# Optimization experiments

Measured on AMD Instinct MI355X. Metric: run time of the kernel, lower is better.

## Reference

```python
import jax, jax.numpy as jnp
import numpy as np

N = 100000
E = 1600000
D_IN = 128
D_H = 128


def _sage_conv(x, src, dst, W_self, W_neigh, b, n_nodes):
    # mean aggregation over in-neighbors: dst receives from src
    gathered = x[src]                                        # [E, D]
    summed = jax.ops.segment_sum(gathered, dst, num_segments=n_nodes)  # [N, D]
    deg = jax.ops.segment_sum(jnp.ones((src.shape[0],), x.dtype), dst,
                              num_segments=n_nodes)          # [N]
    mean_neigh = summed / jnp.maximum(deg, 1.0)[:, None]     # zero-degree -> 0
    return x @ W_self + mean_neigh @ W_neigh + b


def setup_inputs() -> dict:
    key = jax.random.key(0)
    ks = jax.random.split(key, 9)
    s1 = 1.0 / np.sqrt(D_IN)
    s2 = 1.0 / np.sqrt(D_H)
    return {
        "in_feat": jax.random.normal(ks[0], (N, D_IN), jnp.float32),
        "W1_self": jax.random.uniform(ks[1], (D_IN, D_H), jnp.float32, -s1, s1),
        "W1_neigh": jax.random.uniform(ks[2], (D_IN, D_H), jnp.float32, -s1, s1),
        "b1": jnp.zeros((D_H,), jnp.float32),
        "W2_self": jax.random.uniform(ks[3], (D_H, D_H), jnp.float32, -s2, s2),
        "W2_neigh": jax.random.uniform(ks[4], (D_H, D_H), jnp.float32, -s2, s2),
        "b2": jnp.zeros((D_H,), jnp.float32),
        "src": jax.random.randint(ks[5], (E,), 0, N, jnp.int32),
        "dst": jax.random.randint(ks[6], (E,), 0, N, jnp.int32),
    }


def reference(in_feat, W1_self, W1_neigh, b1, W2_self, W2_neigh, b2, src, dst):
    h = _sage_conv(in_feat, src, dst, W1_self, W1_neigh, b1, N)
    h = jax.nn.relu(h)
    h = _sage_conv(h, src, dst, W2_self, W2_neigh, b2, N)
    return h
```

## Files before the change

### kernel.cpp

```cpp
#include <hip/hip_runtime.h>
#include <hip/hip_fp16.h>

#define D 128
#define NBK 512
#define CAP 4544
#define PART_CHUNK 3072

using f32x4  = __attribute__((ext_vector_type(4))) float;
using half8  = __attribute__((ext_vector_type(8))) _Float16;
using short8 = __attribute__((ext_vector_type(8))) short;

#define AS1(p) ((const __attribute__((address_space(1))) void*)(p))
#define AS3(p) ((__attribute__((address_space(3))) void*)(p))

#define FMA_MIX_LO(acc, dw, one) \
    asm("v_fma_mix_f32 %0, %1, %2, %0 op_sel:[0,0,0] op_sel_hi:[1,0,0]" \
        : "+v"(acc) : "v"(dw), "v"(one))
#define FMA_MIX_HI(acc, dw, one) \
    asm("v_fma_mix_f32 %0, %1, %2, %0 op_sel:[1,0,0] op_sel_hi:[1,0,0]" \
        : "+v"(acc) : "v"(dw), "v"(one))

__global__ void prep_k(const float* __restrict__ x, __half* __restrict__ y, int n4,
                       const float* __restrict__ W1s, const float* __restrict__ W1n,
                       const float* __restrict__ W2s, const float* __restrict__ W2n,
                       unsigned short* __restrict__ Wg1, unsigned short* __restrict__ Wg2,
                       float* __restrict__ xpad) {
    int b = blockIdx.x;
    int t = threadIdx.x;
    if (b < 256) {
        if (b == 0 && t < 64) xpad[t] = 0.f;
        int sel = b >> 7;
        int lb  = b & 127;
        const float* Ws = sel ? W2s : W1s;
        const float* Wn = sel ? W2n : W1n;
        unsigned short* Wg = sel ? Wg2 : Wg1;
        int idx = lb * 256 + t;
        int col = idx >> 8;
        int k   = idx & 255;
        float v = (k < 128) ? Ws[k * D + col] : Wn[(k - 128) * D + col];
        _Float16 hv = (_Float16)v;
        _Float16 lv = (_Float16)(v - (float)hv);
        int kc = k >> 5, q = (k >> 3) & 3, j = k & 7;
        Wg[(((kc * 2 + 0) * 4 + q) * 128 + col) * 8 + j] = *(unsigned short*)&hv;
        Wg[(((kc * 2 + 1) * 4 + q) * 128 + col) * 8 + j] = *(unsigned short*)&lv;
        return;
    }
    int i = (b - 256) * 256 + t;
    if (i < n4) {
        float4 v = *(const float4*)(x + (size_t)i * 4);
        __half2 h0 = __floats2half2_rn(v.x, v.y);
        __half2 h1 = __floats2half2_rn(v.z, v.w);
        __half2* o = (__half2*)(y + (size_t)i * 4);
        o[0] = h0; o[1] = h1;
    }
}

__global__ __launch_bounds__(256)
void partition_k(const int* __restrict__ src, const int* __restrict__ dst,
                 int* __restrict__ cursor, unsigned* __restrict__ pairs,
                 int E, int nb, int wmax) {
    __shared__ int hist[NBK];
    __shared__ int gbase[NBK];
    int t = threadIdx.x;
    int e0 = blockIdx.x * PART_CHUNK;
    int e1 = min(E, e0 + PART_CHUNK);
    int e1a = e0 + ((e1 - e0) & ~3);
    for (int b = t; b < nb; b += 256) hist[b] = 0;
    __syncthreads();
    for (int i = e0 + t * 4; i + 3 < e1; i += 1024) {
        int4 d4 = *(const int4*)(dst + i);
        atomicAdd(&hist[d4.x >> 8], 1);
        atomicAdd(&hist[d4.y >> 8], 1);
        atomicAdd(&hist[d4.z >> 8], 1);
        atomicAdd(&hist[d4.w >> 8], 1);
    }
    for (int i = e1a + t; i < e1; i += 256)
        atomicAdd(&hist[dst[i] >> 8], 1);
    __syncthreads();
    for (int b = t; b < nb; b += 256) {
        int c = hist[b];
        int g = b * CAP;
        if (c) g += atomicAdd(&cursor[b], c);
        gbase[b] = g;
        hist[b] = 0;
    }
    __syncthreads();
    for (int i = e0 + t * 4; i + 3 < e1; i += 1024) {
        int4 d4 = *(const int4*)(dst + i);
        int4 s4 = *(const int4*)(src + i);
        int b0 = d4.x >> 8, b1 = d4.y >> 8, b2 = d4.z >> 8, b3 = d4.w >> 8;
        int r0 = atomicAdd(&hist[b0], 1);
        int r1 = atomicAdd(&hist[b1], 1);
        int r2 = atomicAdd(&hist[b2], 1);
        int r3 = atomicAdd(&hist[b3], 1);
        pairs[min(gbase[b0] + r0, wmax)] = ((unsigned)(d4.x & 255) << 17) | (unsigned)s4.x;
        pairs[min(gbase[b1] + r1, wmax)] = ((unsigned)(d4.y & 255) << 17) | (unsigned)s4.y;
        pairs[min(gbase[b2] + r2, wmax)] = ((unsigned)(d4.z & 255) << 17) | (unsigned)s4.z;
        pairs[min(gbase[b3] + r3, wmax)] = ((unsigned)(d4.w & 255) << 17) | (unsigned)s4.w;
    }
    for (int i = e1a + t; i < e1; i += 256) {
        int dd = dst[i];
        int b = dd >> 8;
        int r = atomicAdd(&hist[b], 1);
        pairs[min(gbase[b] + r, wmax)] = ((unsigned)(dd & 255) << 17) | (unsigned)src[i];
    }
}

__global__ __launch_bounds__(1024)
void csr_agg_k(const __half* __restrict__ x, unsigned* pairs,
               const int* __restrict__ cursor, unsigned* __restrict__ offcnt,
               __half* __restrict__ agg, int n) {
    __shared__ int srcs[CAP];
    __shared__ int sh[256];
    __shared__ int hist[256];
    __shared__ int curs[256];
    __shared__ int soff[256];
    __shared__ int scnt[256];
    int t = threadIdx.x;
    int b = blockIdx.x;
    int e0 = b * CAP;
    int cnt = min(cursor[b], CAP);
    int e1 = e0 + cnt;
    if (t < 256) hist[t] = 0;
    __syncthreads();
    for (int i = e0 + t; i < e1; i += 1024)
        atomicAdd(&hist[pairs[i] >> 17], 1);
    __syncthreads();
    int c = 0;
    if (t < 256) { c = hist[t]; sh[t] = c; }
    __syncthreads();
    for (int off = 1; off < 256; off <<= 1) {
        int v = 0;
        if (t >= off && t < 256) v = sh[t - off];
        __syncthreads();
        if (t >= off && t < 256) sh[t] += v;
        __syncthreads();
    }
    if (t < 256) {
        int excl = sh[t] - c;
        curs[t] = excl;
        soff[t] = excl;
        scnt[t] = c;
        int node = (b << 8) + t;
        if (node < n)
            offcnt[node] = ((unsigned)(e0 + excl) << 9) | (unsigned)min(c, 511);
    }
    __syncthreads();
    for (int i = e0 + t; i < e1; i += 1024) {
        unsigned p = pairs[i];
        int pos = atomicAdd(&curs[p >> 17], 1);
        srcs[min(pos, CAP - 1)] = (int)(p & 0x1FFFFu);
    }
    __syncthreads();
    for (int i = t; i < cnt; i += 1024)
        pairs[e0 + i] = (unsigned)srcs[i];
    int lane = t & 63, wv = t >> 6;
    int sg = lane >> 4, sub = lane & 15;
    float one = 1.0f;
    for (int nl = wv; nl < 256; nl += 16) {
        int node = (b << 8) + nl;
        if (node >= n) break;
        int lstart = soff[nl];
        int cnt2 = scnt[nl];
        float acc[8] = {0.f, 0.f, 0.f, 0.f, 0.f, 0.f, 0.f, 0.f};
        for (int base = 0; base < cnt2; base += 64) {
            int valid = min(64, cnt2 - base);
            int s = (lane < valid) ? srcs[lstart + base + lane] : n;
            for (int k0 = 0; k0 < valid; k0 += 16) {
                float4 raw[4];
                #pragma unroll
                for (int u = 0; u < 4; ++u) {
                    int row = __shfl(s, (k0 + 4 * u + sg) & 63);
                    raw[u] = *(const float4*)(x + (size_t)row * D + sub * 8);
                }
                #pragma unroll
                for (int u = 0; u < 4; ++u) {
                    const unsigned* dw = (const unsigned*)&raw[u];
                    #pragma unroll
                    for (int j = 0; j < 4; ++j) {
                        FMA_MIX_LO(acc[2 * j],     dw[j], one);
                        FMA_MIX_HI(acc[2 * j + 1], dw[j], one);
                    }
                }
            }
        }
        #pragma unroll
        for (int j = 0; j < 8; ++j) {
            acc[j] += __shfl(acc[j], lane ^ 16);
            acc[j] += __shfl(acc[j], lane ^ 32);
        }
        if (sg == 0) {
            float inv = 1.0f / fmaxf((float)cnt2, 1.0f);
            union { __half2 h2[4]; short8 s8; } u8;
            #pragma unroll
            for (int j = 0; j < 4; ++j)
                u8.h2[j] = __floats2half2_rn(acc[2 * j] * inv, acc[2 * j + 1] * inv);
            *(short8*)(agg + (size_t)node * D + sub * 8) = u8.s8;
        }
    }
}

__global__ void aggregate_f16_k(const __half* __restrict__ x,
                                const int* __restrict__ edge_src,
                                const unsigned* __restrict__ offcnt,
                                __half* __restrict__ agg, int n) {
    int wid  = (blockIdx.x * blockDim.x + threadIdx.x) >> 6;
    int lane = threadIdx.x & 63;
    if (wid >= n) return;
    int sg  = lane >> 4;
    int sub = lane & 15;
    unsigned pc = offcnt[wid];
    int start = (int)(pc >> 9);
    int cnt   = (int)(pc & 511u);
    float one = 1.0f;
    float acc[8] = {0.f, 0.f, 0.f, 0.f, 0.f, 0.f, 0.f, 0.f};
    for (int base = 0; base < cnt; base += 64) {
        int valid = min(64, cnt - base);
        int s = (lane < valid) ? edge_src[start + base + lane] : n;
        for (int k0 = 0; k0 < valid; k0 += 16) {
            float4 raw[4];
            #pragma unroll
            for (int u = 0; u < 4; ++u) {
                int row = __shfl(s, (k0 + 4 * u + sg) & 63);
                raw[u] = *(const float4*)(x + (size_t)row * D + sub * 8);
            }
            #pragma unroll
            for (int u = 0; u < 4; ++u) {
                const unsigned* dw = (const unsigned*)&raw[u];
                #pragma unroll
                for (int j = 0; j < 4; ++j) {
                    FMA_MIX_LO(acc[2 * j],     dw[j], one);
                    FMA_MIX_HI(acc[2 * j + 1], dw[j], one);
                }
            }
        }
    }
    #pragma unroll
    for (int j = 0; j < 8; ++j) {
        acc[j] += __shfl(acc[j], lane ^ 16);
        acc[j] += __shfl(acc[j], lane ^ 32);
    }
    if (sg == 0) {
        float inv = 1.0f / fmaxf((float)cnt, 1.0f);
        union { __half2 h2[4]; short8 s8; } u;
        #pragma unroll
        for (int j = 0; j < 4; ++j)
            u.h2[j] = __floats2half2_rn(acc[2 * j] * inv, acc[2 * j + 1] * inv);
        *(short8*)(agg + (size_t)wid * D + sub * 8) = u.s8;
    }
}

__global__ __launch_bounds__(512)
void mfma_gemm_k(const _Float16* __restrict__ A0, const _Float16* __restrict__ A1,
                 const unsigned short* __restrict__ Wg,
                 const float* __restrict__ bias,
                 float* __restrict__ C, __half* __restrict__ Ch,
                 int n, int out_mode) {
    __shared__ __align__(16) unsigned short lds_b[8192];
    int t = threadIdx.x;
    int w = t >> 6;
    int l = t & 63;
    int m = l & 15;
    int q = l >> 4;
    int r0 = blockIdx.x * 256 + w * 32;

    f32x4 acc[2][8];
    #pragma unroll
    for (int rt = 0; rt < 2; ++rt)
        #pragma unroll
        for (int ct = 0; ct < 8; ++ct)
            acc[rt][ct] = (f32x4){0.f, 0.f, 0.f, 0.f};

    for (int kc = 0; kc < 8; ++kc) {
        const unsigned short* gk = Wg + (size_t)kc * 8192;
        #pragma unroll
        for (int i = 0; i < 2; ++i) {
            int e = i * 512 + t;
            __builtin_amdgcn_global_load_lds(AS1(gk + e * 8), AS3(lds_b + e * 8), 16, 0, 0);
        }
        const _Float16* __restrict__ A = (kc < 4) ? A0 : A1;
        int ka = (kc & 3) * 32;
        half8 a[2];
        #pragma unroll
        for (int rt = 0; rt < 2; ++rt) {
            int row = r0 + rt * 16 + m;
            half8 v = (half8){0, 0, 0, 0, 0, 0, 0, 0};
            if (row < n) v = *(const half8*)(A + (size_t)row * D + ka + q * 8);
            a[rt] = v;
        }
        __syncthreads();

        #pragma unroll
        for (int ct = 0; ct < 8; ++ct) {
            half8 bh = *(const half8*)&lds_b[(size_t)(q * 128 + ct * 16 + m) * 8];
            half8 bl = *(const half8*)&lds_b[(size_t)((4 + q) * 128 + ct * 16 + m) * 8];
            #pragma unroll
            for (int rt = 0; rt < 2; ++rt) {
                acc[rt][ct] = __builtin_amdgcn_mfma_f32_16x16x32_f16(a[rt], bh, acc[rt][ct], 0, 0, 0);
                acc[rt][ct] = __builtin_amdgcn_mfma_f32_16x16x32_f16(a[rt], bl, acc[rt][ct], 0, 0, 0);
            }
        }
        __syncthreads();
    }

    #pragma unroll
    for (int ct = 0; ct < 8; ++ct) {
        int col = ct * 16 + m;
        float bb = bias[col];
        #pragma unroll
        for (int rt = 0; rt < 2; ++rt) {
            #pragma unroll
            for (int r = 0; r < 4; ++r) {
                int row = r0 + rt * 16 + q * 4 + r;
                if (row < n) {
                    float v = acc[rt][ct][r] + bb;
                    if (out_mode) {
                        v = fmaxf(v, 0.f);
                        Ch[(size_t)row * D + col] = __float2half(v);
                    } else {
                        C[(size_t)row * D + col] = v;
                    }
                }
            }
        }
    }
}

extern "C" void kernel_launch(void* const* d_in, const int* in_sizes, int n_in,
                              void* d_out, int out_size, void* d_ws, size_t ws_size,
                              hipStream_t stream) {
    const float* in_feat = (const float*)d_in[0];
    const float* W1s     = (const float*)d_in[1];
    const float* W1n     = (const float*)d_in[2];
    const float* b1      = (const float*)d_in[3];
    const float* W2s     = (const float*)d_in[4];
    const float* W2n     = (const float*)d_in[5];
    const float* b2      = (const float*)d_in[6];
    const int*   src     = (const int*)d_in[7];
    const int*   dst     = (const int*)d_in[8];

    const int N  = in_sizes[0] / D;
    const int E  = in_sizes[7];
    const int NB = (N + 255) >> 8;

    char* base = (char*)d_ws;
    size_t off = 0;
    __half* agg16 = (__half*)(base + off); off += (size_t)N * D * 2;
    __half* xh16  = (__half*)(base + off); off += ((size_t)N * D + D) * 2;
    unsigned* pairs = (unsigned*)(base + off); off += (size_t)NB * CAP * 4;
    unsigned* offcnt = (unsigned*)(base + off); off += (size_t)N * 4;
    unsigned short* Wg1 = (unsigned short*)(base + off); off += 65536 * 2;
    unsigned short* Wg2 = (unsigned short*)(base + off); off += 65536 * 2;
    int* cursor = (int*)(base + off); off += NBK * 4;

    float* xpad = (float*)(xh16 + (size_t)N * D);

    const int n4 = (N * D) / 4;
    const int xb = (n4 + 255) / 256;
    const int pblk = (E + PART_CHUNK - 1) / PART_CHUNK;

    hipMemsetAsync(cursor, 0, NBK * 4, stream);

    hipLaunchKernelGGL(prep_k, dim3(256 + xb), dim3(256), 0, stream,
                       in_feat, xh16, n4, W1s, W1n, W2s, W2n, Wg1, Wg2, xpad);

    hipLaunchKernelGGL(partition_k, dim3(pblk), dim3(256), 0, stream,
                       src, dst, cursor, pairs, E, NB, NB * CAP - 1);

    const dim3 gemmGrid((N + 255) / 256);
    const dim3 aggGrid(((size_t)N * 64 + 255) / 256);

    hipLaunchKernelGGL(csr_agg_k, dim3(NB), dim3(1024), 0, stream,
                       xh16, pairs, cursor, offcnt, agg16, N);
    hipLaunchKernelGGL(mfma_gemm_k, gemmGrid, dim3(512), 0, stream,
                       (const _Float16*)xh16, (const _Float16*)agg16, Wg1, b1,
                       (float*)nullptr, xh16, N, 1);

    hipLaunchKernelGGL(aggregate_f16_k, aggGrid, dim3(256), 0, stream,
                       xh16, (const int*)pairs, offcnt, agg16, N);
    hipLaunchKernelGGL(mfma_gemm_k, gemmGrid, dim3(512), 0, stream,
                       (const _Float16*)xh16, (const _Float16*)agg16, Wg2, b2,
                       (float*)d_out, (__half*)nullptr, N, 0);
}
```

Baseline: 316.6 us.

## Fuse edge partition into prep kernel and cache pairs in registers in CSR build

```diff
diff --git a/kernel.cpp b/kernel.cpp
--- a/kernel.cpp
+++ b/kernel.cpp
@@ -4,7 +4,7 @@
 #define D 128
 #define NBK 512
 #define CAP 4544
-#define PART_CHUNK 3072
+#define PART_CHUNK 1536
 
 using f32x4  = __attribute__((ext_vector_type(4))) float;
 using half8  = __attribute__((ext_vector_type(8))) _Float16;
@@ -20,17 +20,69 @@
     asm("v_fma_mix_f32 %0, %1, %2, %0 op_sel:[1,0,0] op_sel_hi:[1,0,0]" \
         : "+v"(acc) : "v"(dw), "v"(one))
 
-__global__ void prep_k(const float* __restrict__ x, __half* __restrict__ y, int n4,
-                       const float* __restrict__ W1s, const float* __restrict__ W1n,
-                       const float* __restrict__ W2s, const float* __restrict__ W2n,
-                       unsigned short* __restrict__ Wg1, unsigned short* __restrict__ Wg2,
-                       float* __restrict__ xpad) {
+__global__ __launch_bounds__(256)
+void prep_part_k(const int* __restrict__ src, const int* __restrict__ dst,
+                 int* __restrict__ cursor, unsigned* __restrict__ pairs,
+                 int E, int nb, int wmax, int pblk,
+                 const float* __restrict__ x, __half* __restrict__ y, int n4,
+                 const float* __restrict__ W1s, const float* __restrict__ W1n,
+                 const float* __restrict__ W2s, const float* __restrict__ W2n,
+                 unsigned short* __restrict__ Wg1, unsigned short* __restrict__ Wg2,
+                 float* __restrict__ xpad) {
+    __shared__ int hist[NBK];
+    __shared__ int gbase[NBK];
     int b = blockIdx.x;
     int t = threadIdx.x;
-    if (b < 256) {
-        if (b == 0 && t < 64) xpad[t] = 0.f;
-        int sel = b >> 7;
-        int lb  = b & 127;
+    if (b < pblk) {
+        int e0 = b * PART_CHUNK;
+        int e1 = min(E, e0 + PART_CHUNK);
+        int e1a = e0 + ((e1 - e0) & ~3);
+        for (int i = t; i < nb; i += 256) hist[i] = 0;
+        __syncthreads();
+        for (int i = e0 + t * 4; i + 3 < e1; i += 1024) {
+            int4 d4 = *(const int4*)(dst + i);
+            atomicAdd(&hist[d4.x >> 8], 1);
+            atomicAdd(&hist[d4.y >> 8], 1);
+            atomicAdd(&hist[d4.z >> 8], 1);
+            atomicAdd(&hist[d4.w >> 8], 1);
+        }
+        for (int i = e1a + t; i < e1; i += 256)
+            atomicAdd(&hist[dst[i] >> 8], 1);
+        __syncthreads();
+        for (int i = t; i < nb; i += 256) {
+            int c = hist[i];
+            int g = i * CAP;
+            if (c) g += atomicAdd(&cursor[i], c);
+            gbase[i] = g;
+            hist[i] = 0;
+        }
+        __syncthreads();
+        for (int i = e0 + t * 4; i + 3 < e1; i += 1024) {
+            int4 d4 = *(const int4*)(dst + i);
+            int4 s4 = *(const int4*)(src + i);
+            int b0 = d4.x >> 8, b1 = d4.y >> 8, b2 = d4.z >> 8, b3 = d4.w >> 8;
+            int r0 = atomicAdd(&hist[b0], 1);
+            int r1 = atomicAdd(&hist[b1], 1);
+            int r2 = atomicAdd(&hist[b2], 1);
+            int r3 = atomicAdd(&hist[b3], 1);
+            pairs[min(gbase[b0] + r0, wmax)] = ((unsigned)(d4.x & 255) << 17) | (unsigned)s4.x;
+            pairs[min(gbase[b1] + r1, wmax)] = ((unsigned)(d4.y & 255) << 17) | (unsigned)s4.y;
+            pairs[min(gbase[b2] + r2, wmax)] = ((unsigned)(d4.z & 255) << 17) | (unsigned)s4.z;
+            pairs[min(gbase[b3] + r3, wmax)] = ((unsigned)(d4.w & 255) << 17) | (unsigned)s4.w;
+        }
+        for (int i = e1a + t; i < e1; i += 256) {
+            int dd = dst[i];
+            int bb = dd >> 8;
+            int r = atomicAdd(&hist[bb], 1);
+            pairs[min(gbase[bb] + r, wmax)] = ((unsigned)(dd & 255) << 17) | (unsigned)src[i];
+        }
+        return;
+    }
+    int wb = b - pblk;
+    if (wb < 256) {
+        if (wb == 0 && t < 64) xpad[t] = 0.f;
+        int sel = wb >> 7;
+        int lb  = wb & 127;
         const float* Ws = sel ? W2s : W1s;
         const float* Wn = sel ? W2n : W1n;
         unsigned short* Wg = sel ? Wg2 : Wg1;
@@ -45,64 +97,13 @@
         Wg[(((kc * 2 + 1) * 4 + q) * 128 + col) * 8 + j] = *(unsigned short*)&lv;
         return;
     }
-    int i = (b - 256) * 256 + t;
+    int i = (b - pblk - 256) * 256 + t;
     if (i < n4) {
         float4 v = *(const float4*)(x + (size_t)i * 4);
         __half2 h0 = __floats2half2_rn(v.x, v.y);
         __half2 h1 = __floats2half2_rn(v.z, v.w);
         __half2* o = (__half2*)(y + (size_t)i * 4);
         o[0] = h0; o[1] = h1;
-    }
-}
-
-__global__ __launch_bounds__(256)
-void partition_k(const int* __restrict__ src, const int* __restrict__ dst,
-                 int* __restrict__ cursor, unsigned* __restrict__ pairs,
-                 int E, int nb, int wmax) {
-    __shared__ int hist[NBK];
-    __shared__ int gbase[NBK];
-    int t = threadIdx.x;
-    int e0 = blockIdx.x * PART_CHUNK;
-    int e1 = min(E, e0 + PART_CHUNK);
-    int e1a = e0 + ((e1 - e0) & ~3);
-    for (int b = t; b < nb; b += 256) hist[b] = 0;
-    __syncthreads();
-    for (int i = e0 + t * 4; i + 3 < e1; i += 1024) {
-        int4 d4 = *(const int4*)(dst + i);
-        atomicAdd(&hist[d4.x >> 8], 1);
-        atomicAdd(&hist[d4.y >> 8], 1);
-        atomicAdd(&hist[d4.z >> 8], 1);
-        atomicAdd(&hist[d4.w >> 8], 1);
-    }
-    for (int i = e1a + t; i < e1; i += 256)
-        atomicAdd(&hist[dst[i] >> 8], 1);
-    __syncthreads();
-    for (int b = t; b < nb; b += 256) {
-        int c = hist[b];
-        int g = b * CAP;
-        if (c) g += atomicAdd(&cursor[b], c);
-        gbase[b] = g;
-        hist[b] = 0;
-    }
-    __syncthreads();
-    for (int i = e0 + t * 4; i + 3 < e1; i += 1024) {
-        int4 d4 = *(const int4*)(dst + i);
-        int4 s4 = *(const int4*)(src + i);
-        int b0 = d4.x >> 8, b1 = d4.y >> 8, b2 = d4.z >> 8, b3 = d4.w >> 8;
-        int r0 = atomicAdd(&hist[b0], 1);
-        int r1 = atomicAdd(&hist[b1], 1);
-        int r2 = atomicAdd(&hist[b2], 1);
-        int r3 = atomicAdd(&hist[b3], 1);
-        pairs[min(gbase[b0] + r0, wmax)] = ((unsigned)(d4.x & 255) << 17) | (unsigned)s4.x;
-        pairs[min(gbase[b1] + r1, wmax)] = ((unsigned)(d4.y & 255) << 17) | (unsigned)s4.y;
-        pairs[min(gbase[b2] + r2, wmax)] = ((unsigned)(d4.z & 255) << 17) | (unsigned)s4.z;
-        pairs[min(gbase[b3] + r3, wmax)] = ((unsigned)(d4.w & 255) << 17) | (unsigned)s4.w;
-    }
-    for (int i = e1a + t; i < e1; i += 256) {
-        int dd = dst[i];
-        int b = dd >> 8;
-        int r = atomicAdd(&hist[b], 1);
-        pairs[min(gbase[b] + r, wmax)] = ((unsigned)(dd & 255) << 17) | (unsigned)src[i];
     }
 }
 
@@ -123,8 +124,15 @@
     int e1 = e0 + cnt;
     if (t < 256) hist[t] = 0;
     __syncthreads();
-    for (int i = e0 + t; i < e1; i += 1024)
-        atomicAdd(&hist[pairs[i] >> 17], 1);
+    unsigned pr[5];
+    #pragma unroll
+    for (int j = 0; j < 5; ++j) {
+        int idx = e0 + j * 1024 + t;
+        pr[j] = (idx < e1) ? pairs[idx] : 0xFFFFFFFFu;
+    }
+    #pragma unroll
+    for (int j = 0; j < 5; ++j)
+        if (pr[j] != 0xFFFFFFFFu) atomicAdd(&hist[pr[j] >> 17], 1);
     __syncthreads();
     int c = 0;
     if (t < 256) { c = hist[t]; sh[t] = c; }
@@ -146,11 +154,12 @@
             offcnt[node] = ((unsigned)(e0 + excl) << 9) | (unsigned)min(c, 511);
     }
     __syncthreads();
-    for (int i = e0 + t; i < e1; i += 1024) {
-        unsigned p = pairs[i];
-        int pos = atomicAdd(&curs[p >> 17], 1);
-        srcs[min(pos, CAP - 1)] = (int)(p & 0x1FFFFu);
-    }
+    #pragma unroll
+    for (int j = 0; j < 5; ++j)
+        if (pr[j] != 0xFFFFFFFFu) {
+            int pos = atomicAdd(&curs[pr[j] >> 17], 1);
+            srcs[min(pos, CAP - 1)] = (int)(pr[j] & 0x1FFFFu);
+        }
     __syncthreads();
     for (int i = t; i < cnt; i += 1024)
         pairs[e0 + i] = (unsigned)srcs[i];
@@ -361,11 +370,9 @@
 
     hipMemsetAsync(cursor, 0, NBK * 4, stream);
 
-    hipLaunchKernelGGL(prep_k, dim3(256 + xb), dim3(256), 0, stream,
+    hipLaunchKernelGGL(prep_part_k, dim3(pblk + 256 + xb), dim3(256), 0, stream,
+                       src, dst, cursor, pairs, E, NB, NB * CAP - 1, pblk,
                        in_feat, xh16, n4, W1s, W1n, W2s, W2n, Wg1, Wg2, xpad);
-
-    hipLaunchKernelGGL(partition_k, dim3(pblk), dim3(256), 0, stream,
-                       src, dst, cursor, pairs, E, NB, NB * CAP - 1);
 
     const dim3 gemmGrid((N + 255) / 256);
     const dim3 aggGrid(((size_t)N * 64 + 255) / 256);
```

Measured after the change: 326.1 us. +3.0%, slower.

## Fuse neighbor aggregation with MFMA GEMM per 256-node block

Applied to the files above, without the earlier changes.

```diff
diff --git a/kernel.cpp b/kernel.cpp
--- a/kernel.cpp
+++ b/kernel.cpp
@@ -24,11 +24,11 @@
                        const float* __restrict__ W1s, const float* __restrict__ W1n,
                        const float* __restrict__ W2s, const float* __restrict__ W2n,
                        unsigned short* __restrict__ Wg1, unsigned short* __restrict__ Wg2,
-                       float* __restrict__ xpad) {
+                       float* __restrict__ xpad, float* __restrict__ hpad) {
     int b = blockIdx.x;
     int t = threadIdx.x;
     if (b < 256) {
-        if (b == 0 && t < 64) xpad[t] = 0.f;
+        if (b == 0 && t < 64) { xpad[t] = 0.f; hpad[t] = 0.f; }
         int sel = b >> 7;
         int lb  = b & 127;
         const float* Ws = sel ? W2s : W1s;
@@ -100,17 +100,22 @@
     }
     for (int i = e1a + t; i < e1; i += 256) {
         int dd = dst[i];
-        int b = dd >> 8;
-        int r = atomicAdd(&hist[b], 1);
-        pairs[min(gbase[b] + r, wmax)] = ((unsigned)(dd & 255) << 17) | (unsigned)src[i];
+        int bb = dd >> 8;
+        int r = atomicAdd(&hist[bb], 1);
+        pairs[min(gbase[bb] + r, wmax)] = ((unsigned)(dd & 255) << 17) | (unsigned)src[i];
     }
 }
 
 __global__ __launch_bounds__(1024)
-void csr_agg_k(const __half* __restrict__ x, unsigned* pairs,
-               const int* __restrict__ cursor, unsigned* __restrict__ offcnt,
-               __half* __restrict__ agg, int n) {
+void agg_gemm_k(const __half* __restrict__ xin, unsigned* pairs,
+                const int* __restrict__ cursor, unsigned* __restrict__ offcnt,
+                const unsigned short* __restrict__ Wg,
+                const float* __restrict__ bias,
+                __half* __restrict__ hout, float* __restrict__ fout,
+                int n, int layer1) {
     __shared__ int srcs[CAP];
+    __shared__ __align__(16) __half agg_lds[256][D + 8];
+    __shared__ __align__(16) unsigned short lds_b[8192];
     __shared__ int sh[256];
     __shared__ int hist[256];
     __shared__ int curs[256];
@@ -120,45 +125,65 @@
     int b = blockIdx.x;
     int e0 = b * CAP;
     int cnt = min(cursor[b], CAP);
-    int e1 = e0 + cnt;
-    if (t < 256) hist[t] = 0;
-    __syncthreads();
-    for (int i = e0 + t; i < e1; i += 1024)
-        atomicAdd(&hist[pairs[i] >> 17], 1);
-    __syncthreads();
-    int c = 0;
-    if (t < 256) { c = hist[t]; sh[t] = c; }
-    __syncthreads();
-    for (int off = 1; off < 256; off <<= 1) {
-        int v = 0;
-        if (t >= off && t < 256) v = sh[t - off];
-        __syncthreads();
-        if (t >= off && t < 256) sh[t] += v;
-        __syncthreads();
-    }
-    if (t < 256) {
-        int excl = sh[t] - c;
-        curs[t] = excl;
-        soff[t] = excl;
-        scnt[t] = c;
-        int node = (b << 8) + t;
-        if (node < n)
-            offcnt[node] = ((unsigned)(e0 + excl) << 9) | (unsigned)min(c, 511);
-    }
-    __syncthreads();
-    for (int i = e0 + t; i < e1; i += 1024) {
-        unsigned p = pairs[i];
-        int pos = atomicAdd(&curs[p >> 17], 1);
-        srcs[min(pos, CAP - 1)] = (int)(p & 0x1FFFFu);
-    }
-    __syncthreads();
-    for (int i = t; i < cnt; i += 1024)
-        pairs[e0 + i] = (unsigned)srcs[i];
+    int node0 = b << 8;
+    if (layer1) {
+        if (t < 256) hist[t] = 0;
+        __syncthreads();
+        unsigned pr[5];
+        #pragma unroll
+        for (int j = 0; j < 5; ++j) {
+            int idx = j * 1024 + t;
+            pr[j] = (idx < cnt) ? pairs[e0 + idx] : 0xFFFFFFFFu;
+        }
+        #pragma unroll
+        for (int j = 0; j < 5; ++j)
+            if (pr[j] != 0xFFFFFFFFu) atomicAdd(&hist[pr[j] >> 17], 1);
+        __syncthreads();
+        int c = 0;
+        if (t < 256) { c = hist[t]; sh[t] = c; }
+        __syncthreads();
+        for (int off = 1; off < 256; off <<= 1) {
+            int v = 0;
+            if (t >= off && t < 256) v = sh[t - off];
+            __syncthreads();
+            if (t >= off && t < 256) sh[t] += v;
+            __syncthreads();
+        }
+        if (t < 256) {
+            int excl = sh[t] - c;
+            curs[t] = excl;
+            soff[t] = excl;
+            scnt[t] = c;
+            int node = node0 + t;
+            if (node < n)
+                offcnt[node] = ((unsigned)excl << 9) | (unsigned)min(c, 511);
+        }
+        __syncthreads();
+        #pragma unroll
+        for (int j = 0; j < 5; ++j)
+            if (pr[j] != 0xFFFFFFFFu) {
+                int pos = atomicAdd(&curs[pr[j] >> 17], 1);
+                srcs[min(pos, CAP - 1)] = (int)(pr[j] & 0x1FFFFu);
+            }
+        __syncthreads();
+        for (int i = t; i < cnt; i += 1024)
+            pairs[e0 + i] = (unsigned)srcs[i];
+    } else {
+        for (int i = t; i < cnt; i += 1024)
+            srcs[i] = (int)pairs[e0 + i];
+        if (t < 256) {
+            int node = node0 + t;
+            unsigned pc = (node < n) ? offcnt[node] : 0u;
+            soff[t] = (int)(pc >> 9);
+            scnt[t] = (int)(pc & 511u);
+        }
+        __syncthreads();
+    }
     int lane = t & 63, wv = t >> 6;
     int sg = lane >> 4, sub = lane & 15;
     float one = 1.0f;
     for (int nl = wv; nl < 256; nl += 16) {
-        int node = (b << 8) + nl;
+        int node = node0 + nl;
         if (node >= n) break;
         int lstart = soff[nl];
         int cnt2 = scnt[nl];
@@ -171,7 +196,7 @@
                 #pragma unroll
                 for (int u = 0; u < 4; ++u) {
                     int row = __shfl(s, (k0 + 4 * u + sg) & 63);
-                    raw[u] = *(const float4*)(x + (size_t)row * D + sub * 8);
+                    raw[u] = *(const float4*)(xin + (size_t)row * D + sub * 8);
                 }
                 #pragma unroll
                 for (int u = 0; u < 4; ++u) {
@@ -195,131 +220,52 @@
             #pragma unroll
             for (int j = 0; j < 4; ++j)
                 u8.h2[j] = __floats2half2_rn(acc[2 * j] * inv, acc[2 * j + 1] * inv);
-            *(short8*)(agg + (size_t)node * D + sub * 8) = u8.s8;
-        }
-    }
-}
-
-__global__ void aggregate_f16_k(const __half* __restrict__ x,
-                                const int* __restrict__ edge_src,
-                                const unsigned* __restrict__ offcnt,
-                                __half* __restrict__ agg, int n) {
-    int wid  = (blockIdx.x * blockDim.x + threadIdx.x) >> 6;
-    int lane = threadIdx.x & 63;
-    if (wid >= n) return;
-    int sg  = lane >> 4;
-    int sub = lane & 15;
-    unsigned pc = offcnt[wid];
-    int start = (int)(pc >> 9);
-    int cnt   = (int)(pc & 511u);
-    float one = 1.0f;
-    float acc[8] = {0.f, 0.f, 0.f, 0.f, 0.f, 0.f, 0.f, 0.f};
-    for (int base = 0; base < cnt; base += 64) {
-        int valid = min(64, cnt - base);
-        int s = (lane < valid) ? edge_src[start + base + lane] : n;
-        for (int k0 = 0; k0 < valid; k0 += 16) {
-            float4 raw[4];
-            #pragma unroll
-            for (int u = 0; u < 4; ++u) {
-                int row = __shfl(s, (k0 + 4 * u + sg) & 63);
-                raw[u] = *(const float4*)(x + (size_t)row * D + sub * 8);
-            }
-            #pragma unroll
-            for (int u = 0; u < 4; ++u) {
-                const unsigned* dw = (const unsigned*)&raw[u];
-                #pragma unroll
-                for (int j = 0; j < 4; ++j) {
-                    FMA_MIX_LO(acc[2 * j],     dw[j], one);
-                    FMA_MIX_HI(acc[2 * j + 1], dw[j], one);
-                }
-            }
-        }
-    }
+            *(short8*)(&agg_lds[nl][sub * 8]) = u8.s8;
+        }
+    }
+    __syncthreads();
+    int m = lane & 15, q = lane >> 4;
+    int rowl = wv * 16 + m;
+    int rowg = node0 + rowl;
+    f32x4 acc2[8];
     #pragma unroll
-    for (int j = 0; j < 8; ++j) {
-        acc[j] += __shfl(acc[j], lane ^ 16);
-        acc[j] += __shfl(acc[j], lane ^ 32);
-    }
-    if (sg == 0) {
-        float inv = 1.0f / fmaxf((float)cnt, 1.0f);
-        union { __half2 h2[4]; short8 s8; } u;
-        #pragma unroll
-        for (int j = 0; j < 4; ++j)
-            u.h2[j] = __floats2half2_rn(acc[2 * j] * inv, acc[2 * j + 1] * inv);
-        *(short8*)(agg + (size_t)wid * D + sub * 8) = u.s8;
-    }
-}
-
-__global__ __launch_bounds__(512)
-void mfma_gemm_k(const _Float16* __restrict__ A0, const _Float16* __restrict__ A1,
-                 const unsigned short* __restrict__ Wg,
-                 const float* __restrict__ bias,
-                 float* __restrict__ C, __half* __restrict__ Ch,
-                 int n, int out_mode) {
-    __shared__ __align__(16) unsigned short lds_b[8192];
-    int t = threadIdx.x;
-    int w = t >> 6;
-    int l = t & 63;
-    int m = l & 15;
-    int q = l >> 4;
-    int r0 = blockIdx.x * 256 + w * 32;
-
-    f32x4 acc[2][8];
-    #pragma unroll
-    for (int rt = 0; rt < 2; ++rt)
-        #pragma unroll
-        for (int ct = 0; ct < 8; ++ct)
-            acc[rt][ct] = (f32x4){0.f, 0.f, 0.f, 0.f};
-
+    for (int ct = 0; ct < 8; ++ct) acc2[ct] = (f32x4){0.f, 0.f, 0.f, 0.f};
     for (int kc = 0; kc < 8; ++kc) {
         const unsigned short* gk = Wg + (size_t)kc * 8192;
-        #pragma unroll
-        for (int i = 0; i < 2; ++i) {
-            int e = i * 512 + t;
-            __builtin_amdgcn_global_load_lds(AS1(gk + e * 8), AS3(lds_b + e * 8), 16, 0, 0);
-        }
-        const _Float16* __restrict__ A = (kc < 4) ? A0 : A1;
+        __builtin_amdgcn_global_load_lds(AS1(gk + t * 8), AS3(lds_b + t * 8), 16, 0, 0);
         int ka = (kc & 3) * 32;
-        half8 a[2];
-        #pragma unroll
-        for (int rt = 0; rt < 2; ++rt) {
-            int row = r0 + rt * 16 + m;
-            half8 v = (half8){0, 0, 0, 0, 0, 0, 0, 0};
-            if (row < n) v = *(const half8*)(A + (size_t)row * D + ka + q * 8);
-            a[rt] = v;
-        }
-        __syncthreads();
-
+        half8 a;
+        if (kc < 4) {
+            a = (half8){0, 0, 0, 0, 0, 0, 0, 0};
+            if (rowg < n)
+                a = *(const half8*)((const _Float16*)xin + (size_t)rowg * D + ka + q * 8);
+        } else {
+            a = *(const half8*)(&agg_lds[rowl][ka + q * 8]);
+        }
+        __syncthreads();
         #pragma unroll
         for (int ct = 0; ct < 8; ++ct) {
             half8 bh = *(const half8*)&lds_b[(size_t)(q * 128 + ct * 16 + m) * 8];
             half8 bl = *(const half8*)&lds_b[(size_t)((4 + q) * 128 + ct * 16 + m) * 8];
-            #pragma unroll
-            for (int rt = 0; rt < 2; ++rt) {
-                acc[rt][ct] = __builtin_amdgcn_mfma_f32_16x16x32_f16(a[rt], bh, acc[rt][ct], 0, 0, 0);
-                acc[rt][ct] = __builtin_amdgcn_mfma_f32_16x16x32_f16(a[rt], bl, acc[rt][ct], 0, 0, 0);
-            }
-        }
-        __syncthreads();
-    }
-
+            acc2[ct] = __builtin_amdgcn_mfma_f32_16x16x32_f16(a, bh, acc2[ct], 0, 0, 0);
+            acc2[ct] = __builtin_amdgcn_mfma_f32_16x16x32_f16(a, bl, acc2[ct], 0, 0, 0);
+        }
+        __syncthreads();
+    }
     #pragma unroll
     for (int ct = 0; ct < 8; ++ct) {
         int col = ct * 16 + m;
         float bb = bias[col];
         #pragma unroll
-        for (int rt = 0; rt < 2; ++rt) {
-            #pragma unroll
-            for (int r = 0; r < 4; ++r) {
-                int row = r0 + rt * 16 + q * 4 + r;
-                if (row < n) {
-                    float v = acc[rt][ct][r] + bb;
-                    if (out_mode) {
-                        v = fmaxf(v, 0.f);
-                        Ch[(size_t)row * D + col] = __float2half(v);
-                    } else {
-                        C[(size_t)row * D + col] = v;
-                    }
+        for (int r = 0; r < 4; ++r) {
+            int row = node0 + wv * 16 + q * 4 + r;
+            if (row < n) {
+                float v = acc2[ct][r] + bb;
+                if (layer1) {
+                    v = fmaxf(v, 0.f);
+                    hout[(size_t)row * D + col] = __float2half(v);
+                } else {
+                    fout[(size_t)row * D + col] = v;
                 }
             }
         }
@@ -345,8 +291,8 @@
 
     char* base = (char*)d_ws;
     size_t off = 0;
-    __half* agg16 = (__half*)(base + off); off += (size_t)N * D * 2;
-    __half* xh16  = (__half*)(base + off); off += ((size_t)N * D + D) * 2;
+    __half* h16  = (__half*)(base + off); off += ((size_t)N * D + D) * 2;
+    __half* xh16 = (__half*)(base + off); off += ((size_t)N * D + D) * 2;
     unsigned* pairs = (unsigned*)(base + off); off += (size_t)NB * CAP * 4;
     unsigned* offcnt = (unsigned*)(base + off); off += (size_t)N * 4;
     unsigned short* Wg1 = (unsigned short*)(base + off); off += 65536 * 2;
@@ -354,6 +300,7 @@
     int* cursor = (int*)(base + off); off += NBK * 4;
 
     float* xpad = (float*)(xh16 + (size_t)N * D);
+    float* hpad = (float*)(h16  + (size_t)N * D);
 
     const int n4 = (N * D) / 4;
     const int xb = (n4 + 255) / 256;
@@ -362,23 +309,16 @@
     hipMemsetAsync(cursor, 0, NBK * 4, stream);
 
     hipLaunchKernelGGL(prep_k, dim3(256 + xb), dim3(256), 0, stream,
-                       in_feat, xh16, n4, W1s, W1n, W2s, W2n, Wg1, Wg2, xpad);
+                       in_feat, xh16, n4, W1s, W1n, W2s, W2n, Wg1, Wg2, xpad, hpad);
 
     hipLaunchKernelGGL(partition_k, dim3(pblk), dim3(256), 0, stream,
                        src, dst, cursor, pairs, E, NB, NB * CAP - 1);
 
-    const dim3 gemmGrid((N + 255) / 256);
-    const dim3 aggGrid(((size_t)N * 64 + 255) / 256);
-
-    hipLaunchKernelGGL(csr_agg_k, dim3(NB), dim3(1024), 0, stream,
-                       xh16, pairs, cursor, offcnt, agg16, N);
-    hipLaunchKernelGGL(mfma_gemm_k, gemmGrid, dim3(512), 0, stream,
-                       (const _Float16*)xh16, (const _Float16*)agg16, Wg1, b1,
-                       (float*)nullptr, xh16, N, 1);
-
-    hipLaunchKernelGGL(aggregate_f16_k, aggGrid, dim3(256), 0, stream,
-                       xh16, (const int*)pairs, offcnt, agg16, N);
-    hipLaunchKernelGGL(mfma_gemm_k, gemmGrid, dim3(512), 0, stream,
-                       (const _Float16*)xh16, (const _Float16*)agg16, Wg2, b2,
-                       (float*)d_out, (__half*)nullptr, N, 0);
+    hipLaunchKernelGGL(agg_gemm_k, dim3(NB), dim3(1024), 0, stream,
+                       xh16, pairs, cursor, offcnt, Wg1, b1,
+                       h16, (float*)nullptr, N, 1);
+
+    hipLaunchKernelGGL(agg_gemm_k, dim3(NB), dim3(1024), 0, stream,
+                       h16, pairs, cursor, offcnt, Wg2, b2,
+                       (__half*)nullptr, (float*)d_out, N, 0);
 }
```

Result: slower. 330.1 us (+4.3%).
